# Kernel tuning notes

Hardware: AMD Instinct MI355X
Metric: run time of the kernel (lower is better)

Reference implementation:

```python
import math
import jax, jax.numpy as jnp
import numpy as np

B, T, C, H, DQK, DV = 2, 2048, 1024, 16, 64, 64


def setup_inputs() -> dict:
    key = jax.random.key(0)
    ks = jax.random.split(key, 5)
    x = jax.random.normal(ks[0], (B, T, C), dtype=jnp.float32)
    # randw: randn(*d) / sqrt(d[-1])
    w_q = jax.random.normal(ks[1], (H, DQK, C), dtype=jnp.float32) / math.sqrt(C)
    w_k = jax.random.normal(ks[2], (H, DQK, C), dtype=jnp.float32) / math.sqrt(C)
    w_v = jax.random.normal(ks[3], (H, DV, C), dtype=jnp.float32) / math.sqrt(C)
    w_o = jax.random.normal(ks[4], (DV * H, C), dtype=jnp.float32) / math.sqrt(C)
    return {"x": x, "w_q": w_q, "w_k": w_k, "w_v": w_v, "w_o": w_o}


def reference(x, w_q, w_k, w_v, w_o):
    # Full-sequence causal forward (bs_q.first == 0, nb == T): caches are
    # fully written in one shot, so they reduce to the plain projections.
    n, t, c = x.shape
    q = jnp.einsum('ntc,hdc->nhtd', x, w_q)
    k = jnp.einsum('ntc,hdc->nhtd', x, w_k)
    v = jnp.einsum('ntc,hdc->nhtd', x, w_v)
    scale = 1.0 / math.sqrt(w_q.shape[1])
    a = jnp.einsum('nhtd,nhsd->nhts', q, k) * scale  # [n,h,t,s]
    causal = jnp.arange(t)[:, None] < jnp.arange(t)[None, :]  # True above diag
    a = jnp.where(causal[None, None, :, :], -jnp.inf, a)
    a = jax.nn.softmax(a, axis=3)
    y = jnp.einsum('nhts,nhsd->nthd', a, v).reshape(n, t, -1)  # [n,t,h*dv]
    return y @ w_o  # cache_y, [n,t,c]
```

## Files before the change

### kernel.cpp

```cpp
#include <hip/hip_runtime.h>


typedef short bf16x4 __attribute__((ext_vector_type(4)));
typedef short bf16x8 __attribute__((ext_vector_type(8)));
typedef float f32x4 __attribute__((ext_vector_type(4)));

#define MFMA_BF16 __builtin_amdgcn_mfma_f32_16x16x32_bf16

#define QSCALE 0.18033688011112042f

__device__ __forceinline__ unsigned short f2bf(float f) {
    union { float f; unsigned u; } un; un.f = f;
    unsigned r = un.u + 0x7fffu + ((un.u >> 16) & 1u);
    return (unsigned short)(r >> 16);
}
__device__ __forceinline__ unsigned pk2(float a, float b) {
    return (unsigned)f2bf(a) | ((unsigned)f2bf(b) << 16);
}
__device__ __forceinline__ unsigned pk2t(float a, float b) {
    union { float f; unsigned u; } ua, ub; ua.f = a; ub.f = b;
    return (ua.u >> 16) | (ub.u & 0xffff0000u);
}
__device__ __forceinline__ void gload16(const void* g, void* l) {
    __builtin_amdgcn_global_load_lds(
        (const __attribute__((address_space(1))) unsigned int*)g,
        (__attribute__((address_space(3))) unsigned int*)l, 16, 0, 0);
}

__global__ __launch_bounds__(256) void prep(
    const float* __restrict__ x, const float* __restrict__ wq,
    const float* __restrict__ wk, const float* __restrict__ wv,
    const float* __restrict__ wo,
    unsigned short* __restrict__ x16, unsigned short* __restrict__ wq16,
    unsigned short* __restrict__ wk16, unsigned short* __restrict__ wv16,
    unsigned short* __restrict__ wot)
{
    const int bid = blockIdx.x;
    if (bid < 3584) {
        const float* s; unsigned short* d; int off;
        if (bid < 2048)      { s = x;  d = x16;  off = bid * 2048; }
        else if (bid < 2560) { s = wq; d = wq16; off = (bid - 2048) * 2048; }
        else if (bid < 3072) { s = wk; d = wk16; off = (bid - 2560) * 2048; }
        else                 { s = wv; d = wv16; off = (bid - 3072) * 2048; }
        int i = off + threadIdx.x * 8;
        float4 f0 = *(const float4*)&s[i], f1 = *(const float4*)&s[i + 4];
        uint4 o;
        o.x = pk2(f0.x, f0.y); o.y = pk2(f0.z, f0.w);
        o.z = pk2(f1.x, f1.y); o.w = pk2(f1.z, f1.w);
        *(uint4*)&d[i] = o;
    } else {
        __shared__ unsigned short t[64 * 72];
        const int b2 = bid - 3584;
        const int k0 = (b2 & 15) << 6, n0 = (b2 >> 4) << 6;
        const int r = threadIdx.x >> 2, cg = (threadIdx.x & 3) << 4;
        const float* src = &wo[(k0 + r) * 1024 + n0 + cg];
        #pragma unroll
        for (int j = 0; j < 16; j += 4) {
            float4 f = *(const float4*)&src[j];
            t[(cg + j + 0) * 72 + r] = f2bf(f.x);
            t[(cg + j + 1) * 72 + r] = f2bf(f.y);
            t[(cg + j + 2) * 72 + r] = f2bf(f.z);
            t[(cg + j + 3) * 72 + r] = f2bf(f.w);
        }
        __syncthreads();
        unsigned short* dst = &wot[(n0 + r) * 1024 + k0 + cg];
        unsigned short* tr = &t[r * 72 + cg];
        unsigned v[16];
        #pragma unroll
        for (int j = 0; j < 16; ++j) v[j] = tr[j];
        uint4 o0, o1;
        o0.x = v[0] | (v[1] << 16);   o0.y = v[2] | (v[3] << 16);
        o0.z = v[4] | (v[5] << 16);   o0.w = v[6] | (v[7] << 16);
        o1.x = v[8] | (v[9] << 16);   o1.y = v[10] | (v[11] << 16);
        o1.z = v[12] | (v[13] << 16); o1.w = v[14] | (v[15] << 16);
        *(uint4*)&dst[0] = o0;
        *(uint4*)&dst[8] = o1;
    }
}

__device__ __forceinline__ void gemm_body(
    const unsigned short* __restrict__ A, const unsigned short* __restrict__ Bm,
    void* __restrict__ C, int m0, int n0, int mode, int ldc, float sc)
{
    __shared__ unsigned short sa[128 * 64];
    __shared__ unsigned short sb[128 * 64];
    const int tid = threadIdx.x, wave = tid >> 6, lane = tid & 63;
    const int l15 = lane & 15, l4 = lane >> 4;
    const int wm = (wave >> 1) << 6, wn = (wave & 1) << 6;
    const int lrow = lane >> 3, lcb = (lane & 7) << 3;

    f32x4 acc[4][4] = {};

    for (int k0 = 0; k0 < 1024; k0 += 64) {
        #pragma unroll
        for (int i = 0; i < 4; ++i) {
            int rbase = i * 32 + wave * 8;
            gload16(&A[(size_t)(m0 + rbase + lrow) * 1024 + k0 + lcb], &sa[rbase * 64]);
            gload16(&Bm[(size_t)(n0 + rbase + lrow) * 1024 + k0 + lcb], &sb[rbase * 64]);
        }
        __syncthreads();
        #pragma unroll
        for (int ks = 0; ks < 2; ++ks) {
            bf16x8 af[4], bf[4];
            #pragma unroll
            for (int i = 0; i < 4; ++i)
                af[i] = *(const bf16x8*)&sa[(wm + i * 16 + l15) * 64 + ks * 32 + l4 * 8];
            #pragma unroll
            for (int j = 0; j < 4; ++j)
                bf[j] = *(const bf16x8*)&sb[(wn + j * 16 + l15) * 64 + ks * 32 + l4 * 8];
            #pragma unroll
            for (int i = 0; i < 4; ++i)
                #pragma unroll
                for (int j = 0; j < 4; ++j)
                    acc[i][j] = MFMA_BF16(af[i], bf[j], acc[i][j], 0, 0, 0);
        }
        __syncthreads();
    }

    #pragma unroll
    for (int i = 0; i < 4; ++i)
        #pragma unroll
        for (int j = 0; j < 4; ++j)
            #pragma unroll
            for (int r = 0; r < 4; ++r) {
                int row = m0 + wm + i * 16 + l4 * 4 + r;
                int col = n0 + wn + j * 16 + l15;
                float val = acc[i][j][r];
                if (mode == 0) {
                    int nb = row >> 11, t = row & 2047;
                    int hh = col >> 6, dd = col & 63;
                    ((unsigned short*)C)[(((nb << 4) + hh) * 2048 + t) * 64 + dd] =
                        f2bf(val * sc);
                } else if (mode == 1) {
                    ((float*)C)[(size_t)row * ldc + col] = val;
                } else {
                    ((unsigned short*)C)[(size_t)row * ldc + col] = f2bf(val);
                }
            }
}

__global__ __launch_bounds__(256) void proj(
    const unsigned short* __restrict__ x16,
    const unsigned short* __restrict__ wq16,
    const unsigned short* __restrict__ wk16,
    const unsigned short* __restrict__ wv16,
    unsigned short* __restrict__ qbuf,
    unsigned short* __restrict__ kbuf,
    unsigned short* __restrict__ vtb)
{
    const int bid = blockIdx.x;
    if (bid < 512) {
        int m0 = (bid & 31) << 7;
        int n0g = (bid >> 5) << 7;
        if (n0g < 1024)
            gemm_body(x16, wq16, qbuf, m0, n0g, 0, 0, QSCALE);
        else
            gemm_body(x16, wk16, kbuf, m0, n0g - 1024, 0, 0, 1.0f);
    } else {
        int v = bid - 512;
        gemm_body(wv16, x16, vtb, (v & 7) << 7, (v >> 3) << 7, 2, 4096, 1.0f);
    }
}

__global__ __launch_bounds__(256) void outp(
    const unsigned short* __restrict__ ybuf,
    const unsigned short* __restrict__ wot,
    float* __restrict__ out)
{
    __shared__ unsigned short sa[64 * 64];
    __shared__ unsigned short sb[128 * 64];
    const int tid = threadIdx.x, wave = tid >> 6, lane = tid & 63;
    const int l15 = lane & 15, l4 = lane >> 4;
    const int bid = blockIdx.x;
    const int m0 = (bid & 63) << 6, n0 = (bid >> 6) << 7;
    const int lrow = lane >> 3, lcb = (lane & 7) << 3;

    f32x4 acc[8] = {};

    for (int k0 = 0; k0 < 1024; k0 += 64) {
        #pragma unroll
        for (int i = 0; i < 2; ++i) {
            int rbase = i * 32 + wave * 8;
            gload16(&ybuf[(size_t)(m0 + rbase + lrow) * 1024 + k0 + lcb], &sa[rbase * 64]);
        }
        #pragma unroll
        for (int i = 0; i < 4; ++i) {
            int rbase = i * 32 + wave * 8;
            gload16(&wot[(size_t)(n0 + rbase + lrow) * 1024 + k0 + lcb], &sb[rbase * 64]);
        }
        __syncthreads();
        #pragma unroll
        for (int ks = 0; ks < 2; ++ks) {
            bf16x8 af = *(const bf16x8*)&sa[(wave * 16 + l15) * 64 + ks * 32 + l4 * 8];
            #pragma unroll
            for (int j = 0; j < 8; ++j) {
                bf16x8 bf = *(const bf16x8*)&sb[(j * 16 + l15) * 64 + ks * 32 + l4 * 8];
                acc[j] = MFMA_BF16(af, bf, acc[j], 0, 0, 0);
            }
        }
        __syncthreads();
    }

    #pragma unroll
    for (int j = 0; j < 8; ++j)
        #pragma unroll
        for (int r = 0; r < 4; ++r) {
            int row = m0 + wave * 16 + l4 * 4 + r;
            int col = n0 + j * 16 + l15;
            out[(size_t)row * 1024 + col] = acc[j][r];
        }
}

__global__ __launch_bounds__(256) void attn(
    const unsigned short* __restrict__ q,
    const unsigned short* __restrict__ k,
    const unsigned short* __restrict__ vt,
    unsigned short* __restrict__ y)
{
    constexpr int P = 72;
    __shared__ unsigned short sk[64 * P];
    __shared__ unsigned short sv[64 * P];
    const int tid = threadIdx.x, wave = tid >> 6, lane = tid & 63;
    const int l15 = lane & 15, l4 = lane >> 4;
    const int bid = blockIdx.x;
    const int qtt = (bid < 512) ? (31 - (bid >> 5)) : ((bid - 512) >> 5);
    const int bh = bid & 31;
    const int nb = bh >> 4, hh = bh & 15;
    const int q0 = qtt << 6;
    const size_t base = (size_t)bh << 17;

    bf16x8 qf[2];
    #pragma unroll
    for (int ks = 0; ks < 2; ++ks)
        qf[ks] = *(const bf16x8*)
            &q[base + (size_t)(q0 + wave * 16 + l15) * 64 + ks * 32 + l4 * 8];

    float l_sum = 0.f;
    f32x4 acc[4] = {};

    const int nst = qtt + 1;
    for (int st = 0; st < nst; ++st) {
        const int s0 = st << 6;
        for (int vv = tid; vv < 512; vv += 256) {
            int row = vv >> 3, col = (vv & 7) << 3;
            *(uint4*)&sk[row * P + col] =
                *(const uint4*)&k[base + (size_t)((s0 + row) << 6) + col];
            *(uint4*)&sv[row * P + col] =
                *(const uint4*)&vt[(size_t)((hh << 6) + row) * 4096 + (nb << 11) + s0 + col];
        }
        __syncthreads();

        f32x4 s_acc[4] = {};
        #pragma unroll
        for (int ks = 0; ks < 2; ++ks)
            #pragma unroll
            for (int ns = 0; ns < 4; ++ns) {
                bf16x8 kf = *(const bf16x8*)&sk[(ns * 16 + l15) * P + ks * 32 + l4 * 8];
                s_acc[ns] = MFMA_BF16(kf, qf[ks], s_acc[ns], 0, 0, 0);
            }

        if (st == qtt) {
            const int ql = wave * 16 + l15;
            #pragma unroll
            for (int ns = 0; ns < 4; ++ns) {
                #pragma unroll
                for (int r = 0; r < 4; ++r)
                    if (ns * 16 + l4 * 4 + r > ql) s_acc[ns][r] = -1e30f;
            }
        }

        float pe[4][4];
        #pragma unroll
        for (int ns = 0; ns < 4; ++ns) {
            #pragma unroll
            for (int r = 0; r < 4; ++r) pe[ns][r] = exp2f(s_acc[ns][r]);
            l_sum += (pe[ns][0] + pe[ns][1]) + (pe[ns][2] + pe[ns][3]);
        }

        #pragma unroll
        for (int ks = 0; ks < 2; ++ks) {
            uint4 pw;
            pw.x = pk2t(pe[2 * ks][0], pe[2 * ks][1]);
            pw.y = pk2t(pe[2 * ks][2], pe[2 * ks][3]);
            pw.z = pk2t(pe[2 * ks + 1][0], pe[2 * ks + 1][1]);
            pw.w = pk2t(pe[2 * ks + 1][2], pe[2 * ks + 1][3]);
            bf16x8 pf = *(bf16x8*)&pw;
            #pragma unroll
            for (int ds = 0; ds < 4; ++ds) {
                const unsigned short* vrow = &sv[(ds * 16 + l15) * P + ks * 32 + l4 * 4];
                bf16x4 lo = *(const bf16x4*)vrow;
                bf16x4 hi = *(const bf16x4*)(vrow + 16);
                bf16x8 vf = __builtin_shufflevector(lo, hi, 0, 1, 2, 3, 4, 5, 6, 7);
                acc[ds] = MFMA_BF16(vf, pf, acc[ds], 0, 0, 0);
            }
        }
        __syncthreads();
    }

    l_sum += __shfl_xor(l_sum, 16);
    l_sum += __shfl_xor(l_sum, 32);
    const float rl = __builtin_amdgcn_rcpf(l_sum);

    const size_t rowbase =
        ((size_t)((nb << 11) + q0 + wave * 16 + l15) << 10) + (hh << 6) + l4 * 4;
    #pragma unroll
    for (int ds = 0; ds < 4; ++ds) {
        uint2 o;
        o.x = pk2(acc[ds][0] * rl, acc[ds][1] * rl);
        o.y = pk2(acc[ds][2] * rl, acc[ds][3] * rl);
        *(uint2*)&y[rowbase + ds * 16] = o;
    }
}

extern "C" void kernel_launch(void* const* d_in, const int* in_sizes, int n_in,
                              void* d_out, int out_size, void* d_ws, size_t ws_size,
                              hipStream_t stream) {
    const float* x  = (const float*)d_in[0];
    const float* wq = (const float*)d_in[1];
    const float* wk = (const float*)d_in[2];
    const float* wv = (const float*)d_in[3];
    const float* wo = (const float*)d_in[4];
    float* out = (float*)d_out;

    const size_t M1 = 1u << 20;
    unsigned short* x16  = (unsigned short*)d_ws;
    unsigned short* wq16 = x16 + 4 * M1;
    unsigned short* wk16 = wq16 + M1;
    unsigned short* wv16 = wk16 + M1;
    unsigned short* wot  = wv16 + M1;
    unsigned short* qbuf = wot + M1;
    unsigned short* kbuf = qbuf + 4 * M1;
    unsigned short* vtb  = kbuf + 4 * M1;
    unsigned short* ybuf = vtb + 4 * M1;

    dim3 blk(256);
    prep<<<3840, blk, 0, stream>>>(x, wq, wk, wv, wo, x16, wq16, wk16, wv16, wot);
    proj<<<768, blk, 0, stream>>>(x16, wq16, wk16, wv16, qbuf, kbuf, vtb);
    attn<<<1024, blk, 0, stream>>>(qbuf, kbuf, vtb, ybuf);
    outp<<<512, blk, 0, stream>>>(ybuf, wot, out);
}
```

Measured before the change: 210.4 us.

## Double-buffer K/V tiles in attention and shrink output-projection tile width

The attention kernel now prefetches the next K and V^T tiles into registers while the current tile is being computed, and stores them into a second shared-memory buffer. This hides global-load latency behind the MFMA work and drops one barrier per iteration. Separately, the output projection tile goes from 64x128 to 64x64 with twice as many blocks, which raises parallelism but reloads the A tile more often. The double buffer doubles attention's LDS footprint, which may lower occupancy.

```diff
diff --git a/kernel.cpp b/kernel.cpp
--- a/kernel.cpp
+++ b/kernel.cpp
@@ -168,24 +168,20 @@
     float* __restrict__ out)
 {
     __shared__ unsigned short sa[64 * 64];
-    __shared__ unsigned short sb[128 * 64];
+    __shared__ unsigned short sb[64 * 64];
     const int tid = threadIdx.x, wave = tid >> 6, lane = tid & 63;
     const int l15 = lane & 15, l4 = lane >> 4;
     const int bid = blockIdx.x;
-    const int m0 = (bid & 63) << 6, n0 = (bid >> 6) << 7;
+    const int m0 = (bid & 63) << 6, n0 = (bid >> 6) << 6;
     const int lrow = lane >> 3, lcb = (lane & 7) << 3;
 
-    f32x4 acc[8] = {};
+    f32x4 acc[4] = {};
 
     for (int k0 = 0; k0 < 1024; k0 += 64) {
         #pragma unroll
         for (int i = 0; i < 2; ++i) {
             int rbase = i * 32 + wave * 8;
             gload16(&ybuf[(size_t)(m0 + rbase + lrow) * 1024 + k0 + lcb], &sa[rbase * 64]);
-        }
-        #pragma unroll
-        for (int i = 0; i < 4; ++i) {
-            int rbase = i * 32 + wave * 8;
             gload16(&wot[(size_t)(n0 + rbase + lrow) * 1024 + k0 + lcb], &sb[rbase * 64]);
         }
         __syncthreads();
@@ -193,7 +189,7 @@
         for (int ks = 0; ks < 2; ++ks) {
             bf16x8 af = *(const bf16x8*)&sa[(wave * 16 + l15) * 64 + ks * 32 + l4 * 8];
             #pragma unroll
-            for (int j = 0; j < 8; ++j) {
+            for (int j = 0; j < 4; ++j) {
                 bf16x8 bf = *(const bf16x8*)&sb[(j * 16 + l15) * 64 + ks * 32 + l4 * 8];
                 acc[j] = MFMA_BF16(af, bf, acc[j], 0, 0, 0);
             }
@@ -202,7 +198,7 @@
     }
 
     #pragma unroll
-    for (int j = 0; j < 8; ++j)
+    for (int j = 0; j < 4; ++j)
         #pragma unroll
         for (int r = 0; r < 4; ++r) {
             int row = m0 + wave * 16 + l4 * 4 + r;
@@ -218,8 +214,8 @@
     unsigned short* __restrict__ y)
 {
     constexpr int P = 72;
-    __shared__ unsigned short sk[64 * P];
-    __shared__ unsigned short sv[64 * P];
+    __shared__ unsigned short sk[2][64 * P];
+    __shared__ unsigned short sv[2][64 * P];
     const int tid = threadIdx.x, wave = tid >> 6, lane = tid & 63;
     const int l15 = lane & 15, l4 = lane >> 4;
     const int bid = blockIdx.x;
@@ -229,6 +225,11 @@
     const int q0 = qtt << 6;
     const size_t base = (size_t)bh << 17;
 
+    const int r0 = tid >> 3, c0 = (tid & 7) << 3;
+    const unsigned short* kg = &k[base + ((size_t)r0 << 6) + c0];
+    const unsigned short* vg = &vt[(size_t)((hh << 6) + r0) * 4096 + (nb << 11) + c0];
+    const int lk0 = r0 * P + c0, lk1 = (r0 + 32) * P + c0;
+
     bf16x8 qf[2];
     #pragma unroll
     for (int ks = 0; ks < 2; ++ks)
@@ -239,23 +240,35 @@
     f32x4 acc[4] = {};
 
     const int nst = qtt + 1;
+
+    {
+        uint4 ka = *(const uint4*)(kg);
+        uint4 kb = *(const uint4*)(kg + (32 << 6));
+        uint4 va = *(const uint4*)(vg);
+        uint4 vb = *(const uint4*)(vg + 32 * 4096);
+        *(uint4*)&sk[0][lk0] = ka;  *(uint4*)&sk[0][lk1] = kb;
+        *(uint4*)&sv[0][lk0] = va;  *(uint4*)&sv[0][lk1] = vb;
+    }
+    __syncthreads();
+
     for (int st = 0; st < nst; ++st) {
-        const int s0 = st << 6;
-        for (int vv = tid; vv < 512; vv += 256) {
-            int row = vv >> 3, col = (vv & 7) << 3;
-            *(uint4*)&sk[row * P + col] =
-                *(const uint4*)&k[base + (size_t)((s0 + row) << 6) + col];
-            *(uint4*)&sv[row * P + col] =
-                *(const uint4*)&vt[(size_t)((hh << 6) + row) * 4096 + (nb << 11) + s0 + col];
-        }
-        __syncthreads();
+        const int cur = st & 1;
+        const bool more = (st + 1) < nst;
+        uint4 ka, kb, va, vb;
+        if (more) {
+            const int s1 = (st + 1) << 6;
+            ka = *(const uint4*)(kg + ((size_t)s1 << 6));
+            kb = *(const uint4*)(kg + ((size_t)(s1 + 32) << 6));
+            va = *(const uint4*)(vg + s1);
+            vb = *(const uint4*)(vg + 32 * 4096 + s1);
+        }
 
         f32x4 s_acc[4] = {};
         #pragma unroll
         for (int ks = 0; ks < 2; ++ks)
             #pragma unroll
             for (int ns = 0; ns < 4; ++ns) {
-                bf16x8 kf = *(const bf16x8*)&sk[(ns * 16 + l15) * P + ks * 32 + l4 * 8];
+                bf16x8 kf = *(const bf16x8*)&sk[cur][(ns * 16 + l15) * P + ks * 32 + l4 * 8];
                 s_acc[ns] = MFMA_BF16(kf, qf[ks], s_acc[ns], 0, 0, 0);
             }
 
@@ -287,12 +300,19 @@
             bf16x8 pf = *(bf16x8*)&pw;
             #pragma unroll
             for (int ds = 0; ds < 4; ++ds) {
-                const unsigned short* vrow = &sv[(ds * 16 + l15) * P + ks * 32 + l4 * 4];
+                const unsigned short* vrow =
+                    &sv[cur][(ds * 16 + l15) * P + ks * 32 + l4 * 4];
                 bf16x4 lo = *(const bf16x4*)vrow;
                 bf16x4 hi = *(const bf16x4*)(vrow + 16);
                 bf16x8 vf = __builtin_shufflevector(lo, hi, 0, 1, 2, 3, 4, 5, 6, 7);
                 acc[ds] = MFMA_BF16(vf, pf, acc[ds], 0, 0, 0);
             }
+        }
+
+        if (more) {
+            const int nxt = 1 - cur;
+            *(uint4*)&sk[nxt][lk0] = ka;  *(uint4*)&sk[nxt][lk1] = kb;
+            *(uint4*)&sv[nxt][lk0] = va;  *(uint4*)&sv[nxt][lk1] = vb;
         }
         __syncthreads();
     }
@@ -337,5 +357,5 @@
     prep<<<3840, blk, 0, stream>>>(x, wq, wk, wv, wo, x16, wq16, wk16, wv16, wot);
     proj<<<768, blk, 0, stream>>>(x16, wq16, wk16, wv16, qbuf, kbuf, vtb);
     attn<<<1024, blk, 0, stream>>>(qbuf, kbuf, vtb, ybuf);
-    outp<<<512, blk, 0, stream>>>(ybuf, wot, out);
-}
+    outp<<<1024, blk, 0, stream>>>(ybuf, wot, out);
+}
```

Measured after the change: 193.1 us. -8.2%, faster.
